# Kernel optimization log

Hardware: AMD Instinct MI355X
Metric: run time of the kernel (lower is better)

## Reference

```python
import jax, jax.numpy as jnp
import numpy as np

D_MODEL = 1024
N_HEADS = 16
HEAD_DIM = D_MODEL // N_HEADS


def setup_inputs() -> dict:
    key = jax.random.key(0)
    ks = jax.random.split(key, 9)
    scale = 1.0 / np.sqrt(D_MODEL)
    x = jax.random.normal(ks[0], (2, 2048, D_MODEL), dtype=jnp.float32)
    Wq = jax.random.normal(ks[1], (D_MODEL, D_MODEL), dtype=jnp.float32) * scale
    bq = jnp.zeros((D_MODEL,), dtype=jnp.float32)
    Wk = jax.random.normal(ks[2], (D_MODEL, D_MODEL), dtype=jnp.float32) * scale
    bk = jnp.zeros((D_MODEL,), dtype=jnp.float32)
    Wv = jax.random.normal(ks[3], (D_MODEL, D_MODEL), dtype=jnp.float32) * scale
    bv = jnp.zeros((D_MODEL,), dtype=jnp.float32)
    Wo = jax.random.normal(ks[4], (D_MODEL, D_MODEL), dtype=jnp.float32) * scale
    bo = jnp.zeros((D_MODEL,), dtype=jnp.float32)
    return {"x": x, "Wq": Wq, "bq": bq, "Wk": Wk, "bk": bk,
            "Wv": Wv, "bv": bv, "Wo": Wo, "bo": bo}


def reference(x, Wq, bq, Wk, bk, Wv, bv, Wo, bo):
    B, S, D = x.shape
    H, Hd = N_HEADS, HEAD_DIM
    # projections, reshape to [B, H, S, Hd]
    def split_heads(t):
        return t.reshape(B, S, H, Hd).transpose(0, 2, 1, 3)
    q = split_heads(x @ Wq.T + bq)
    k = split_heads(x @ Wk.T + bk)
    v = split_heads(x @ Wv.T + bv)
    scores = jnp.einsum('bhqd,bhkd->bhqk', q, k) / jnp.sqrt(jnp.float32(Hd))
    attn = jax.nn.softmax(scores, axis=-1)  # dropout is identity in eval mode
    ctx = jnp.einsum('bhqk,bhkd->bhqd', attn, v)
    ctx = ctx.transpose(0, 2, 1, 3).reshape(B, S, D)
    out = ctx @ Wo.T + bo
    return out, attn
```

## Files before the change

### kernel.cpp

```cpp
#include <hip/hip_runtime.h>
#include <hip/hip_bf16.h>

using bf16 = __hip_bfloat16;
typedef __attribute__((ext_vector_type(8))) short bf16x8;
typedef __attribute__((ext_vector_type(4))) float f32x4;
typedef __attribute__((ext_vector_type(4))) short sh4_t;

#define DEVI static __device__ __forceinline__

DEVI short f2b(float x) {
    bf16 h = __float2bfloat16(x);
    return __builtin_bit_cast(short, h);
}

__global__ __launch_bounds__(256) void mha_cvt(const float* __restrict__ src,
                                               bf16* __restrict__ dst, int n) {
    int i = (blockIdx.x * 256 + threadIdx.x) * 4;
    if (i < n) {
        float4 v = *(const float4*)(src + i);
        sh4_t o;
        o.x = f2b(v.x); o.y = f2b(v.y); o.z = f2b(v.z); o.w = f2b(v.w);
        *(sh4_t*)((short*)dst + i) = o;
    }
}

template<int EPI>
__global__ __launch_bounds__(256)
void mha_gemm_bt(const bf16* __restrict__ A, const bf16* __restrict__ B, int K,
                 const float* __restrict__ b0, const float* __restrict__ b1,
                 const float* __restrict__ b2,
                 bf16* __restrict__ Qb, bf16* __restrict__ Kb,
                 bf16* __restrict__ Vb, float* __restrict__ Cout) {
    __shared__ __align__(16) bf16 As[128 * 64];
    __shared__ __align__(16) bf16 Bs[128 * 64];
    const int tid  = threadIdx.x;
    const int wave = tid >> 6, lane = tid & 63;
    const int l16  = lane & 15, lg = lane >> 4;
    const int rb   = blockIdx.y * 128;
    const int cb   = blockIdx.x * 128;
    const int wr   = (wave >> 1) * 64, wc = (wave & 1) * 64;

    f32x4 acc[4][4] = {};

    const int srow = wave * 32 + (lane >> 3);
    const int scol = (lane & 7) * 8;

    for (int k0 = 0; k0 < K; k0 += 64) {
        if (k0) __syncthreads();
#pragma unroll
        for (int i = 0; i < 4; ++i) {
            __builtin_amdgcn_global_load_lds(
                (const __attribute__((address_space(1))) void*)
                    (A + (size_t)(rb + srow + i * 8) * K + k0 + scol),
                (__attribute__((address_space(3))) void*)(As + wave * 2048 + i * 512),
                16, 0, 0);
        }
#pragma unroll
        for (int i = 0; i < 4; ++i) {
            __builtin_amdgcn_global_load_lds(
                (const __attribute__((address_space(1))) void*)
                    (B + (size_t)(cb + srow + i * 8) * K + k0 + scol),
                (__attribute__((address_space(3))) void*)(Bs + wave * 2048 + i * 512),
                16, 0, 0);
        }
        __syncthreads();
#pragma unroll
        for (int ks = 0; ks < 2; ++ks) {
            bf16x8 af[4], bfv[4];
#pragma unroll
            for (int m = 0; m < 4; ++m)
                af[m] = *(const bf16x8*)(As + (wr + m * 16 + l16) * 64 + ks * 32 + lg * 8);
#pragma unroll
            for (int n = 0; n < 4; ++n)
                bfv[n] = *(const bf16x8*)(Bs + (wc + n * 16 + l16) * 64 + ks * 32 + lg * 8);
#pragma unroll
            for (int m = 0; m < 4; ++m)
#pragma unroll
                for (int n = 0; n < 4; ++n)
                    acc[m][n] = __builtin_amdgcn_mfma_f32_16x16x32_bf16(
                        af[m], bfv[n], acc[m][n], 0, 0, 0);
        }
    }

    if constexpr (EPI == 0) {
#pragma unroll
        for (int nn = 0; nn < 4; ++nn) {
            int c  = cb + wc + nn * 16 + l16;
            float bias = (c < 1024) ? b0[c] : (c < 2048 ? b1[c - 1024] : b2[c - 2048]);
            int sel = c >> 10, cc = c & 1023, hh = cc >> 6, dd = cc & 63;
#pragma unroll
            for (int mm = 0; mm < 4; ++mm) {
#pragma unroll
                for (int j = 0; j < 4; ++j) {
                    int r  = rb + wr + mm * 16 + lg * 4 + j;
                    int bb = r >> 11, ss = r & 2047;
                    bf16 hv = __float2bfloat16(acc[mm][nn][j] + bias);
                    size_t bhx = (size_t)(bb * 16 + hh);
                    if (sel == 0)      Qb[(bhx * 2048 + ss) * 64 + dd] = hv;
                    else if (sel == 1) Kb[(bhx * 2048 + ss) * 64 + dd] = hv;
                    else               Vb[(bhx * 2048 + ss) * 64 + dd] = hv;
                }
            }
        }
    } else {
#pragma unroll
        for (int mm = 0; mm < 4; ++mm)
#pragma unroll
            for (int nn = 0; nn < 4; ++nn)
#pragma unroll
                for (int j = 0; j < 4; ++j) {
                    int r = rb + wr + mm * 16 + lg * 4 + j;
                    int c = cb + wc + nn * 16 + l16;
                    Cout[(size_t)r * 1024 + c] = acc[mm][nn][j] + b0[c];
                }
    }
}

__global__ __launch_bounds__(256)
void mha_vtr(const bf16* __restrict__ Vb, bf16* __restrict__ VTb) {
    __shared__ bf16 T[64][68];
    const int kt = blockIdx.x, bh = blockIdx.y, tid = threadIdx.x;
    const int r = tid >> 3, c = (tid & 7) * 8;
    const bf16* src = Vb + ((size_t)bh * 2048 + (size_t)kt * 64) * 64;
#pragma unroll
    for (int i = 0; i < 2; ++i)
        *(bf16x8*)&T[r + i * 32][c] = *(const bf16x8*)(src + (size_t)(r + i * 32) * 64 + c);
    __syncthreads();
    bf16* dst = VTb + (size_t)bh * 64 * 2048 + (size_t)kt * 64;
#pragma unroll
    for (int i = 0; i < 2; ++i) {
        int d = r + i * 32;
        bf16x8 v;
#pragma unroll
        for (int z = 0; z < 8; ++z)
            v[z] = __builtin_bit_cast(short, T[c + z][d]);
        *(bf16x8*)(dst + (size_t)d * 2048 + c) = v;
    }
}

__global__ __launch_bounds__(256)
void mha_attn(const bf16* __restrict__ Qb, const bf16* __restrict__ Kb,
              const bf16* __restrict__ VTb, float* __restrict__ attnO,
              bf16* __restrict__ ctxb) {
    __shared__ __align__(16) bf16 Ks[64 * 72];
    __shared__ __align__(16) bf16 Vs[64 * 72];
    __shared__ __align__(16) float Pf[4][16][68];

    const int tid = threadIdx.x, wave = tid >> 6, lane = tid & 63;
    const int l16 = lane & 15, lg = lane >> 4;
    const int qt = blockIdx.x, bh = blockIdx.y;
    const int b = bh >> 4, h = bh & 15;
    const bf16* Qh = Qb + (size_t)bh * 2048 * 64;
    const bf16* Kh = Kb + (size_t)bh * 2048 * 64;
    const bf16* Vh = VTb + (size_t)bh * 64 * 2048;

    bf16x8 aq[2];
    {
        int qrow = qt * 64 + wave * 16 + l16;
        aq[0] = *(const bf16x8*)(Qh + (size_t)qrow * 64 + lg * 8);
        aq[1] = *(const bf16x8*)(Qh + (size_t)qrow * 64 + 32 + lg * 8);
    }
    const int sr = tid >> 3;
    const int sc = (tid & 7) * 8;

    float l[4] = {0.f, 0.f, 0.f, 0.f};

    for (int kt = 0; kt < 32; ++kt) {
        __syncthreads();
#pragma unroll
        for (int i = 0; i < 2; ++i)
            *(bf16x8*)(Ks + (sr + i * 32) * 72 + sc) =
                *(const bf16x8*)(Kh + (size_t)(kt * 64 + sr + i * 32) * 64 + sc);
        __syncthreads();

        f32x4 s[4] = {};
#pragma unroll
        for (int ks = 0; ks < 2; ++ks)
#pragma unroll
            for (int n = 0; n < 4; ++n) {
                bf16x8 bk = *(const bf16x8*)(Ks + (n * 16 + l16) * 72 + ks * 32 + lg * 8);
                s[n] = __builtin_amdgcn_mfma_f32_16x16x32_bf16(aq[ks], bk, s[n], 0, 0, 0);
            }
#pragma unroll
        for (int n = 0; n < 4; ++n)
#pragma unroll
            for (int j = 0; j < 4; ++j)
                l[j] += __expf(s[n][j] * 0.125f);
    }
#pragma unroll
    for (int msk = 1; msk < 16; msk <<= 1)
#pragma unroll
        for (int j = 0; j < 4; ++j)
            l[j] += __shfl_xor(l[j], msk);
    float linv[4];
#pragma unroll
    for (int j = 0; j < 4; ++j) linv[j] = 1.0f / l[j];

    f32x4 oacc[4] = {};

    for (int kt = 0; kt < 32; ++kt) {
        __syncthreads();
#pragma unroll
        for (int i = 0; i < 2; ++i) {
            *(bf16x8*)(Ks + (sr + i * 32) * 72 + sc) =
                *(const bf16x8*)(Kh + (size_t)(kt * 64 + sr + i * 32) * 64 + sc);
            *(bf16x8*)(Vs + (sr + i * 32) * 72 + sc) =
                *(const bf16x8*)(Vh + (size_t)(sr + i * 32) * 2048 + kt * 64 + sc);
        }
        __syncthreads();

        f32x4 s[4] = {};
#pragma unroll
        for (int ks = 0; ks < 2; ++ks)
#pragma unroll
            for (int n = 0; n < 4; ++n) {
                bf16x8 bk = *(const bf16x8*)(Ks + (n * 16 + l16) * 72 + ks * 32 + lg * 8);
                s[n] = __builtin_amdgcn_mfma_f32_16x16x32_bf16(aq[ks], bk, s[n], 0, 0, 0);
            }
#pragma unroll
        for (int n = 0; n < 4; ++n)
#pragma unroll
            for (int j = 0; j < 4; ++j)
                Pf[wave][lg * 4 + j][n * 16 + l16] = __expf(s[n][j] * 0.125f) * linv[j];
        float* aB = attnO + ((size_t)bh * 2048 + qt * 64 + wave * 16) * 2048 + (size_t)kt * 64;
#pragma unroll
        for (int i = 0; i < 4; ++i) {
            int row = i * 4 + lg;
            f32x4 v = *(const f32x4*)&Pf[wave][row][l16 * 4];
            *(f32x4*)(aB + (size_t)row * 2048 + l16 * 4) = v;
        }
#pragma unroll
        for (int ks = 0; ks < 2; ++ks) {
            f32x4 plo = *(const f32x4*)&Pf[wave][l16][ks * 32 + lg * 8];
            f32x4 phi = *(const f32x4*)&Pf[wave][l16][ks * 32 + lg * 8 + 4];
            bf16x8 pa;
#pragma unroll
            for (int z = 0; z < 4; ++z) {
                pa[z]     = f2b(plo[z]);
                pa[z + 4] = f2b(phi[z]);
            }
#pragma unroll
            for (int n = 0; n < 4; ++n) {
                bf16x8 bv = *(const bf16x8*)(Vs + (n * 16 + l16) * 72 + ks * 32 + lg * 8);
                oacc[n] = __builtin_amdgcn_mfma_f32_16x16x32_bf16(pa, bv, oacc[n], 0, 0, 0);
            }
        }
    }
    int token0 = b * 2048 + qt * 64 + wave * 16;
#pragma unroll
    for (int n = 0; n < 4; ++n)
#pragma unroll
        for (int j = 0; j < 4; ++j)
            ctxb[(size_t)(token0 + lg * 4 + j) * 1024 + h * 64 + n * 16 + l16] =
                __float2bfloat16(oacc[n][j]);
}

extern "C" void kernel_launch(void* const* d_in, const int* in_sizes, int n_in,
                              void* d_out, int out_size, void* d_ws, size_t ws_size,
                              hipStream_t stream) {
    const float* x  = (const float*)d_in[0];
    const float* Wq = (const float*)d_in[1];
    const float* bq = (const float*)d_in[2];
    const float* Wk = (const float*)d_in[3];
    const float* bk = (const float*)d_in[4];
    const float* Wv = (const float*)d_in[5];
    const float* bv = (const float*)d_in[6];
    const float* Wo = (const float*)d_in[7];
    const float* bo = (const float*)d_in[8];

    float* out  = (float*)d_out;
    float* attn = out + (size_t)4194304;

    char* ws = (char*)d_ws;
    bf16* xb   = (bf16*)(ws);
    bf16* wqkv = (bf16*)(ws + (size_t)( 8 << 20));
    bf16* wob  = (bf16*)(ws + (size_t)(14 << 20));
    bf16* Qb   = (bf16*)(ws + (size_t)(16 << 20));
    bf16* Kb   = (bf16*)(ws + (size_t)(24 << 20));
    bf16* VTb  = (bf16*)(ws + (size_t)(32 << 20));
    bf16* ctxb = (bf16*)(ws + (size_t)(40 << 20));
    bf16* Vb   = ctxb;

    mha_cvt<<<4096, 256, 0, stream>>>(x, xb, 4194304);
    mha_cvt<<<1024, 256, 0, stream>>>(Wq, wqkv,           1048576);
    mha_cvt<<<1024, 256, 0, stream>>>(Wk, wqkv + 1048576, 1048576);
    mha_cvt<<<1024, 256, 0, stream>>>(Wv, wqkv + 2097152, 1048576);
    mha_cvt<<<1024, 256, 0, stream>>>(Wo, wob,            1048576);

    mha_gemm_bt<0><<<dim3(24, 32), 256, 0, stream>>>(
        xb, wqkv, 1024, bq, bk, bv, Qb, Kb, Vb, nullptr);

    mha_vtr<<<dim3(32, 32), 256, 0, stream>>>(Vb, VTb);

    mha_attn<<<dim3(32, 32), 256, 0, stream>>>(Qb, Kb, VTb, attn, ctxb);

    mha_gemm_bt<1><<<dim3(8, 32), 256, 0, stream>>>(
        ctxb, wob, 1024, bo, nullptr, nullptr, nullptr, nullptr, nullptr, out);
}
```

Before: 733.9 us.

## Merge conversion launches, stage QKV epilogue via LDS, remap attention blocks per XCD

The five fp32-to-bf16 conversion launches become one kernel that picks its source and destination from the block index. The QKV GEMM epilogue now writes bias-added bf16 results into shared memory, then stores 16-byte vectors to the head-split layout instead of scattered 2-byte stores. The attention grid is flattened so that blocks sharing a (batch, head) land on the same XCD, aiming for better L2 reuse of K and V. In exchange, the epilogue adds extra barriers and reuses the GEMM's shared memory.

```diff
diff --git a/kernel.cpp b/kernel.cpp
--- a/kernel.cpp
+++ b/kernel.cpp
@@ -13,15 +13,28 @@
     return __builtin_bit_cast(short, h);
 }
 
-__global__ __launch_bounds__(256) void mha_cvt(const float* __restrict__ src,
-                                               bf16* __restrict__ dst, int n) {
-    int i = (blockIdx.x * 256 + threadIdx.x) * 4;
-    if (i < n) {
-        float4 v = *(const float4*)(src + i);
-        sh4_t o;
-        o.x = f2b(v.x); o.y = f2b(v.y); o.z = f2b(v.z); o.w = f2b(v.w);
-        *(sh4_t*)((short*)dst + i) = o;
-    }
+__global__ __launch_bounds__(256)
+void mha_cvt_all(const float* __restrict__ x,  const float* __restrict__ wq,
+                 const float* __restrict__ wk, const float* __restrict__ wv,
+                 const float* __restrict__ wo,
+                 bf16* __restrict__ xb, bf16* __restrict__ wqkv,
+                 bf16* __restrict__ wob) {
+    int b = blockIdx.x;
+    const float* src;
+    bf16* dst;
+    int lb;
+    if (b < 4096) { src = x; dst = xb; lb = b; }
+    else {
+        int w = b - 4096, wi = w >> 10;
+        lb  = w & 1023;
+        src = wi == 0 ? wq : wi == 1 ? wk : wi == 2 ? wv : wo;
+        dst = wi == 3 ? wob : wqkv + (size_t)wi * 1048576;
+    }
+    int i = (lb * 256 + threadIdx.x) * 4;
+    float4 v = *(const float4*)(src + i);
+    sh4_t o;
+    o.x = f2b(v.x); o.y = f2b(v.y); o.z = f2b(v.z); o.w = f2b(v.w);
+    *(sh4_t*)((short*)dst + i) = o;
 }
 
 template<int EPI>
@@ -31,8 +44,9 @@
                  const float* __restrict__ b2,
                  bf16* __restrict__ Qb, bf16* __restrict__ Kb,
                  bf16* __restrict__ Vb, float* __restrict__ Cout) {
-    __shared__ __align__(16) bf16 As[128 * 64];
-    __shared__ __align__(16) bf16 Bs[128 * 64];
+    __shared__ __align__(16) bf16 smem[16384];
+    bf16* As = smem;
+    bf16* Bs = smem + 8192;
     const int tid  = threadIdx.x;
     const int wave = tid >> 6, lane = tid & 63;
     const int l16  = lane & 15, lg = lane >> 4;
@@ -83,23 +97,37 @@
     }
 
     if constexpr (EPI == 0) {
-#pragma unroll
-        for (int nn = 0; nn < 4; ++nn) {
-            int c  = cb + wc + nn * 16 + l16;
-            float bias = (c < 1024) ? b0[c] : (c < 2048 ? b1[c - 1024] : b2[c - 2048]);
-            int sel = c >> 10, cc = c & 1023, hh = cc >> 6, dd = cc & 63;
-#pragma unroll
-            for (int mm = 0; mm < 4; ++mm) {
-#pragma unroll
-                for (int j = 0; j < 4; ++j) {
-                    int r  = rb + wr + mm * 16 + lg * 4 + j;
-                    int bb = r >> 11, ss = r & 2047;
-                    bf16 hv = __float2bfloat16(acc[mm][nn][j] + bias);
-                    size_t bhx = (size_t)(bb * 16 + hh);
-                    if (sel == 0)      Qb[(bhx * 2048 + ss) * 64 + dd] = hv;
-                    else if (sel == 1) Kb[(bhx * 2048 + ss) * 64 + dd] = hv;
-                    else               Vb[(bhx * 2048 + ss) * 64 + dd] = hv;
-                }
+        const int sel = cb >> 10;
+        const int h0  = (cb & 1023) >> 6;
+        const float* bp = sel == 0 ? b0 : sel == 1 ? b1 : b2;
+        bf16* dstp      = sel == 0 ? Qb : sel == 1 ? Kb : Vb;
+        float bias[4];
+#pragma unroll
+        for (int nn = 0; nn < 4; ++nn)
+            bias[nn] = bp[(cb + wc + nn * 16 + l16) & 1023];
+        bf16* Ct = smem;
+        for (int h2 = 0; h2 < 2; ++h2) {
+            __syncthreads();
+            if ((wave >> 1) == h2) {
+#pragma unroll
+                for (int mm = 0; mm < 4; ++mm)
+#pragma unroll
+                    for (int nn = 0; nn < 4; ++nn)
+#pragma unroll
+                        for (int j = 0; j < 4; ++j)
+                            Ct[(mm * 16 + lg * 4 + j) * 136 + wc + nn * 16 + l16] =
+                                __float2bfloat16(acc[mm][nn][j] + bias[nn]);
+            }
+            __syncthreads();
+#pragma unroll
+            for (int i = 0; i < 4; ++i) {
+                int c = tid + 256 * i;
+                int lrow = c >> 4, cc = (c & 15) * 8;
+                bf16x8 v = *(const bf16x8*)(Ct + lrow * 136 + cc);
+                int rg = rb + h2 * 64 + lrow;
+                int bb = rg >> 11, ss = rg & 2047;
+                int hh = h0 + (cc >> 6), dd = cc & 63;
+                *(bf16x8*)(dstp + (((size_t)(bb * 16 + hh)) * 2048 + ss) * 64 + dd) = v;
             }
         }
     } else {
@@ -148,7 +176,10 @@
 
     const int tid = threadIdx.x, wave = tid >> 6, lane = tid & 63;
     const int l16 = lane & 15, lg = lane >> 4;
-    const int qt = blockIdx.x, bh = blockIdx.y;
+    const int L = blockIdx.x;
+    const int sL = L >> 3, xcd = L & 7;
+    const int bh = xcd + 8 * (sL >> 5);
+    const int qt = sL & 31;
     const int b = bh >> 4, h = bh & 15;
     const bf16* Qh = Qb + (size_t)bh * 2048 * 64;
     const bf16* Kh = Kb + (size_t)bh * 2048 * 64;
@@ -281,18 +312,14 @@
     bf16* ctxb = (bf16*)(ws + (size_t)(40 << 20));
     bf16* Vb   = ctxb;
 
-    mha_cvt<<<4096, 256, 0, stream>>>(x, xb, 4194304);
-    mha_cvt<<<1024, 256, 0, stream>>>(Wq, wqkv,           1048576);
-    mha_cvt<<<1024, 256, 0, stream>>>(Wk, wqkv + 1048576, 1048576);
-    mha_cvt<<<1024, 256, 0, stream>>>(Wv, wqkv + 2097152, 1048576);
-    mha_cvt<<<1024, 256, 0, stream>>>(Wo, wob,            1048576);
+    mha_cvt_all<<<8192, 256, 0, stream>>>(x, Wq, Wk, Wv, Wo, xb, wqkv, wob);
 
     mha_gemm_bt<0><<<dim3(24, 32), 256, 0, stream>>>(
         xb, wqkv, 1024, bq, bk, bv, Qb, Kb, Vb, nullptr);
 
     mha_vtr<<<dim3(32, 32), 256, 0, stream>>>(Vb, VTb);
 
-    mha_attn<<<dim3(32, 32), 256, 0, stream>>>(Qb, Kb, VTb, attn, ctxb);
+    mha_attn<<<1024, 256, 0, stream>>>(Qb, Kb, VTb, attn, ctxb);
 
     mha_gemm_bt<1><<<dim3(8, 32), 256, 0, stream>>>(
         ctxb, wob, 1024, bo, nullptr, nullptr, nullptr, nullptr, nullptr, out);
```

Result: no change. 734.2 us (+0.0%).
